# Kernel tuning notes

Measured on AMD Instinct MI355X. Metric: run time of the kernel, lower is better.

Reference implementation:

```python
import jax, jax.numpy as jnp
import numpy as np
import math

N_HEADS = 8
Q_DIM = 512          # number of query tokens (first Q_DIM rows of q)
INPUT_DIM = 512
EMBED_DIM = 512
HEAD_DIM = EMBED_DIM // N_HEADS  # key_dim == val_dim == 64
BATCH = 8
TOTAL_TOKENS = 4096  # Q_DIM queries + 3584 context tokens
NORM = 1.0 / math.sqrt(HEAD_DIM)


def setup_inputs() -> dict:
    key = jax.random.key(0)
    k1, k2, k3, k4, k5 = jax.random.split(key, 5)
    stdv = 1.0 / math.sqrt(HEAD_DIM)
    return {
        "q": jax.random.normal(k1, (BATCH, TOTAL_TOKENS, INPUT_DIM), dtype=jnp.float32),
        "W_query": jax.random.uniform(k2, (N_HEADS, INPUT_DIM, HEAD_DIM), minval=-stdv, maxval=stdv, dtype=jnp.float32),
        "W_key": jax.random.uniform(k3, (N_HEADS, INPUT_DIM, HEAD_DIM), minval=-stdv, maxval=stdv, dtype=jnp.float32),
        "W_val": jax.random.uniform(k4, (N_HEADS, INPUT_DIM, HEAD_DIM), minval=-stdv, maxval=stdv, dtype=jnp.float32),
        "W_out": jax.random.uniform(k5, (N_HEADS, HEAD_DIM, EMBED_DIM), minval=-1.0 / math.sqrt(EMBED_DIM), maxval=1.0 / math.sqrt(EMBED_DIM), dtype=jnp.float32),
    }


def reference(q, W_query, W_key, W_val, W_out):
    # Split packed input: first Q_DIM tokens are queries, rest are context.
    q_ = q[:, :Q_DIM, :]          # [b, nq, d_in]
    h = q[:, Q_DIM:, :]           # [b, g, d_in]
    Q = jnp.einsum('bqi,hik->hbqk', q_, W_query)   # [h, b, nq, dk]
    K = jnp.einsum('bgi,hik->hbgk', h, W_key)      # [h, b, g, dk]
    V = jnp.einsum('bgi,hiv->hbgv', h, W_val)      # [h, b, g, dv]
    compat = NORM * jnp.einsum('hbqk,hbgk->hbqg', Q, K)  # [h, b, nq, g]
    attn = jax.nn.softmax(compat, axis=-1)
    heads = jnp.einsum('hbqg,hbgv->hbqv', attn, V)       # [h, b, nq, dv]
    out = jnp.einsum('hbqv,hve->bqe', heads, W_out)      # [b, nq, embed]
    return out
```

## Files before the change

### kernel.cpp

```cpp
#include <hip/hip_runtime.h>

typedef _Float16 f16;
typedef _Float16 f16x4 __attribute__((ext_vector_type(4)));
typedef _Float16 f16x8 __attribute__((ext_vector_type(8)));
typedef float    f32x4 __attribute__((ext_vector_type(4)));

#define MFMA(a,b,c) __builtin_amdgcn_mfma_f32_16x16x32_f16(a,b,c,0,0,0)

#if __has_builtin(__builtin_amdgcn_exp2f)
#define EXP2(x) __builtin_amdgcn_exp2f(x)
#else
#define EXP2(x) exp2f(x)
#endif

__device__ __forceinline__ void gld16(const void* g, void* l) {
  typedef __attribute__((address_space(1))) unsigned GU;
  typedef __attribute__((address_space(3))) unsigned LU;
  __builtin_amdgcn_global_load_lds((GU*)g, (LU*)l, 16, 0, 0);
}

__global__ __launch_bounds__(256) void transp_w(
    const float* __restrict__ Wq, const float* __restrict__ Wk,
    const float* __restrict__ Wv, const float* __restrict__ Wo,
    f16* __restrict__ Wqt, f16* __restrict__ Wkt, f16* __restrict__ Wvt,
    f16* __restrict__ Wot)
{
  __shared__ float T[64 * 65];
  int bid = blockIdx.x, t = threadIdx.x;
  int mat = bid >> 6;
  int i0 = (bid & 7) * 64, c0 = ((bid >> 3) & 7) * 64;
  const float* src; f16* dst; float scale = 1.f;
  if      (mat == 0) { src = Wq; dst = Wqt; scale = 0.125f * 1.4426950408889634f; }
  else if (mat == 1) { src = Wk; dst = Wkt; }
  else if (mat == 2) { src = Wv; dst = Wvt; }
  else               { src = Wo; dst = Wot; }
#pragma unroll
  for (int p = 0; p < 4; ++p) {
    int row = p * 16 + (t >> 4), col = (t & 15) * 4;
    const float* a = (mat < 3)
        ? src + ((c0 >> 6) * 512 + i0 + row) * 64 + col
        : src + (i0 + row) * 512 + c0 + col;
    f32x4 v = *(const f32x4*)a;
    T[row * 65 + col + 0] = v[0] * scale;
    T[row * 65 + col + 1] = v[1] * scale;
    T[row * 65 + col + 2] = v[2] * scale;
    T[row * 65 + col + 3] = v[3] * scale;
  }
  __syncthreads();
#pragma unroll
  for (int p = 0; p < 16; ++p) {
    int cc = (t >> 6) * 16 + p, ii = t & 63;
    dst[(c0 + cc) * 512 + i0 + ii] = (f16)T[ii * 65 + cc];
  }
}

__global__ __launch_bounds__(256, 3) void proj_kernel(
    const float* __restrict__ q,
    const f16* __restrict__ Wqt, const f16* __restrict__ Wkt, const f16* __restrict__ Wvt,
    f16* __restrict__ Qh, f16* __restrict__ Kh, f16* __restrict__ Vtb)
{
  __shared__ f16 Asl[2][4096];
  __shared__ f16 Bsl[2][4096];

  int bid0 = blockIdx.x;
  int tile = (bid0 & 7) * 240 + (bid0 >> 3);

  int tid = threadIdx.x, l = tid & 63, w = tid >> 6;
  int wr = w >> 1, wc = w & 1;

  bool qmode = tile < 128;
  int rt, colbase, vmode = 0;
  const f16* Wt;
  if (qmode) {
    rt = tile >> 2; colbase = (tile & 3) * 128; Wt = Wqt;
  } else {
    int t2 = tile - 128; rt = t2 >> 3; int cc = t2 & 7;
    if (cc < 4) { Wt = Wkt; colbase = cc * 128; }
    else        { Wt = Wvt; colbase = (cc - 4) * 128; vmode = 1; }
  }
  int gbase, bidx;
  if (qmode) { bidx = rt >> 2; gbase = bidx * 4096 + (rt & 3) * 128; }
  else       { bidx = rt / 28; gbase = bidx * 4096 + 512 + (rt * 128 - bidx * 3584); }

  const float* asrc[2];
  const f16*   bsrc[2];
  int ldst[2];
#pragma unroll
  for (int j = 0; j < 2; ++j) {
    int s = tid + j * 256;
    int r = s >> 2;
    int c = (s & 3) ^ ((r >> 1) & 3);
    asrc[j] = q  + (size_t)(gbase + r) * 512 + c * 8;
    bsrc[j] = Wt + (size_t)(colbase + r) * 512 + c * 8;
    ldst[j] = (j * 256 + w * 64) * 8;
  }
  int awrow = tid >> 1, awh = tid & 1;
  int awo0 = awrow * 64 + (((awh * 2 + 0) ^ ((awrow >> 1) & 3)) << 4);
  int awo1 = awrow * 64 + (((awh * 2 + 1) ^ ((awrow >> 1) & 3)) << 4);
  const float* awsrc = q + (size_t)(gbase + awrow) * 512 + awh * 16;

  int aro[4], bro[4];
#pragma unroll
  for (int i = 0; i < 4; ++i) {
    int ra = wr * 64 + i * 16 + (l & 15);
    aro[i] = ra * 64 + ((((l >> 4)) ^ ((ra >> 1) & 3)) << 4);
    int rb = wc * 64 + i * 16 + (l & 15);
    bro[i] = rb * 64 + ((((l >> 4)) ^ ((rb >> 1) & 3)) << 4);
  }

  const f32x4 z4 = {0.f, 0.f, 0.f, 0.f};
  f32x4 acc[4][4];
#pragma unroll
  for (int i = 0; i < 4; ++i)
#pragma unroll
    for (int j = 0; j < 4; ++j) acc[i][j] = z4;

  f32x4 ar0, ar1, ar2, ar3;

  ar0 = *(const f32x4*)(awsrc + 0);
  ar1 = *(const f32x4*)(awsrc + 4);
  ar2 = *(const f32x4*)(awsrc + 8);
  ar3 = *(const f32x4*)(awsrc + 12);
  gld16(bsrc[0], &Bsl[0][ldst[0]]);
  gld16(bsrc[1], &Bsl[0][ldst[1]]);
  {
    f16x8 h0, h1;
#pragma unroll
    for (int e = 0; e < 4; ++e) { h0[e] = (f16)ar0[e]; h0[4+e] = (f16)ar1[e];
                                  h1[e] = (f16)ar2[e]; h1[4+e] = (f16)ar3[e]; }
    *(f16x8*)((char*)&Asl[0][0] + awo0) = h0;
    *(f16x8*)((char*)&Asl[0][0] + awo1) = h1;
  }
  __syncthreads();

  for (int ks = 0; ks < 16; ++ks) {
    int cur = ks & 1;
    if (ks < 15) {
      int k0 = (ks + 1) * 32;
      ar0 = *(const f32x4*)(awsrc + k0 + 0);
      ar1 = *(const f32x4*)(awsrc + k0 + 4);
      ar2 = *(const f32x4*)(awsrc + k0 + 8);
      ar3 = *(const f32x4*)(awsrc + k0 + 12);
      gld16(bsrc[0] + k0, &Bsl[cur ^ 1][ldst[0]]);
      gld16(bsrc[1] + k0, &Bsl[cur ^ 1][ldst[1]]);
    }
    const char* AB = (const char*)&Asl[cur][0];
    const char* BB = (const char*)&Bsl[cur][0];
    f16x8 af[4], bf[4];
#pragma unroll
    for (int i = 0; i < 4; ++i) af[i] = *(const f16x8*)(AB + aro[i]);
#pragma unroll
    for (int i = 0; i < 4; ++i) bf[i] = *(const f16x8*)(BB + bro[i]);
#pragma unroll
    for (int mi = 0; mi < 4; ++mi)
#pragma unroll
      for (int ni = 0; ni < 4; ++ni)
        acc[mi][ni] = MFMA(af[mi], bf[ni], acc[mi][ni]);
    if (ks < 15) {
      f16x8 h0, h1;
#pragma unroll
      for (int e = 0; e < 4; ++e) { h0[e] = (f16)ar0[e]; h0[4+e] = (f16)ar1[e];
                                    h1[e] = (f16)ar2[e]; h1[4+e] = (f16)ar3[e]; }
      *(f16x8*)((char*)&Asl[cur ^ 1][0] + awo0) = h0;
      *(f16x8*)((char*)&Asl[cur ^ 1][0] + awo1) = h1;
    }
    __syncthreads();
  }

  if (qmode) {
#pragma unroll
    for (int mi = 0; mi < 4; ++mi) {
      int row = rt * 128 + wr * 64 + mi * 16 + (l >> 4) * 4;
#pragma unroll
      for (int ni = 0; ni < 4; ++ni) {
        int col = colbase + wc * 64 + ni * 16 + (l & 15);
#pragma unroll
        for (int r = 0; r < 4; ++r)
          Qh[(size_t)(row + r) * 512 + col] = (f16)acc[mi][ni][r];
      }
    }
  } else if (!vmode) {
#pragma unroll
    for (int mi = 0; mi < 4; ++mi) {
      int row = rt * 128 + wr * 64 + mi * 16 + (l >> 4) * 4;
#pragma unroll
      for (int ni = 0; ni < 4; ++ni) {
        int col = colbase + wc * 64 + ni * 16 + (l & 15);
#pragma unroll
        for (int r = 0; r < 4; ++r)
          Kh[(size_t)(row + r) * 512 + col] = (f16)acc[mi][ni][r];
      }
    }
  } else {
    int g0 = rt * 128 - bidx * 3584;
#pragma unroll
    for (int mi = 0; mi < 4; ++mi) {
      int g = g0 + wr * 64 + mi * 16 + (l >> 4) * 4;
#pragma unroll
      for (int ni = 0; ni < 4; ++ni) {
        int c4 = colbase + wc * 64 + ni * 16 + (l & 15);
        int hh = c4 >> 6, v = c4 & 63;
        f16x4 o4;
        o4[0] = (f16)acc[mi][ni][0]; o4[1] = (f16)acc[mi][ni][1];
        o4[2] = (f16)acc[mi][ni][2]; o4[3] = (f16)acc[mi][ni][3];
        *(f16x4*)(Vtb + (size_t)((bidx * 8 + hh) * 64 + v) * 3584 + g) = o4;
      }
    }
  }
}

__global__ __launch_bounds__(512, 4) void attn_kernel(
    const f16* __restrict__ Qh, const f16* __restrict__ Kh,
    const f16* __restrict__ Vtb, f16* __restrict__ Opart,
    float* __restrict__ Ml, float* __restrict__ Ll)
{
  __shared__ f16 Klds[2][4096];
  __shared__ f16 Vlds[2][4096];
  __shared__ f16 Plds[8 * 1152];

  int bid = blockIdx.x;
  int seg = bid & 1, qt = (bid >> 1) & 3, h = (bid >> 3) & 7, bb = bid >> 6;
  int q0 = qt * 128;
  int tid = threadIdx.x, l = tid & 63, w = tid >> 6;

  f16x8 qf0, qf1;
  {
    int qrow = q0 + w * 16 + (l & 15);
    const f16* qb = Qh + (bb * 512 + qrow) * 512 + h * 64 + ((l >> 4) * 8);
    qf0 = *(const f16x8*)qb;
    qf1 = *(const f16x8*)(qb + 32);
  }

  bool isK = (w < 4);
  int sdo[2], ssrc[2];
#pragma unroll
  for (int j = 0; j < 2; ++j) {
    int id = (isK ? w : (w - 4)) * 2 + j;
    int rr = id * 8 + (l >> 3);
    int co = ((l & 7) ^ (rr & 7)) * 8;
    sdo[j] = id * 512;
    if (isK) ssrc[j] = (bb * 3584 + seg * 1792 + rr) * 512 + h * 64 + co;
    else     ssrc[j] = ((bb * 8 + h) * 64 + rr) * 3584 + seg * 1792 + co;
  }

  const f32x4 z4 = {0.f, 0.f, 0.f, 0.f};
  f32x4 acco[4];
#pragma unroll
  for (int i = 0; i < 4; ++i) acco[i] = z4;
  float mrow = -1e30f, lrow = 0.f;

  char* PwB = (char*)&Plds[w * 1152];
  int pwbase = (l & 15) * 144 + (l >> 4) * 8;
  int prbase = (l & 15) * 144 + (l >> 4) * 16;

  if (isK) { gld16(Kh + ssrc[0], &Klds[0][sdo[0]]); gld16(Kh + ssrc[1], &Klds[0][sdo[1]]); }
  else     { gld16(Vtb + ssrc[0], &Vlds[0][sdo[0]]); gld16(Vtb + ssrc[1], &Vlds[0][sdo[1]]); }
  __syncthreads();

  int buf = 0;
  for (int it = 0; it < 28; ++it) {
    if (it < 27) {
      int g0 = (it + 1) * 64;
      if (isK) { gld16(Kh + ssrc[0] + g0 * 512, &Klds[buf ^ 1][sdo[0]]);
                 gld16(Kh + ssrc[1] + g0 * 512, &Klds[buf ^ 1][sdo[1]]); }
      else     { gld16(Vtb + ssrc[0] + g0, &Vlds[buf ^ 1][sdo[0]]);
                 gld16(Vtb + ssrc[1] + g0, &Vlds[buf ^ 1][sdo[1]]); }
    }
    const char* KB = (const char*)&Klds[buf][0];
    const char* VB = (const char*)&Vlds[buf][0];

    f32x4 accs[4];
#pragma unroll
    for (int i = 0; i < 4; ++i) accs[i] = z4;
#pragma unroll
    for (int ni = 0; ni < 4; ++ni) {
      int g = ni * 16 + (l & 15);
      const char* rp = KB + g * 128;
      f16x8 k0 = *(const f16x8*)(rp + ((((l >> 4)    ) ^ (g & 7)) << 4));
      f16x8 k1 = *(const f16x8*)(rp + (((4 + (l >> 4)) ^ (g & 7)) << 4));
      accs[ni] = MFMA(k0, qf0, accs[ni]);
      accs[ni] = MFMA(k1, qf1, accs[ni]);
    }

    float n0 = fmaxf(fmaxf(accs[0][0], accs[0][1]), fmaxf(accs[0][2], accs[0][3]));
    float n1 = fmaxf(fmaxf(accs[1][0], accs[1][1]), fmaxf(accs[1][2], accs[1][3]));
    float n2 = fmaxf(fmaxf(accs[2][0], accs[2][1]), fmaxf(accs[2][2], accs[2][3]));
    float n3 = fmaxf(fmaxf(accs[3][0], accs[3][1]), fmaxf(accs[3][2], accs[3][3]));
    float tm = fmaxf(fmaxf(n0, n1), fmaxf(n2, n3));
    tm = fmaxf(tm, __shfl_xor(tm, 16));
    tm = fmaxf(tm, __shfl_xor(tm, 32));
    float mn = fmaxf(mrow, tm);
    float alpha = EXP2(mrow - mn);
    mrow = mn;

    float rs = 0.f;
#pragma unroll
    for (int ni = 0; ni < 4; ++ni) {
      float s0 = EXP2(accs[ni][0] - mrow);
      float s1 = EXP2(accs[ni][1] - mrow);
      float s2 = EXP2(accs[ni][2] - mrow);
      float s3 = EXP2(accs[ni][3] - mrow);
      rs += (s0 + s1) + (s2 + s3);
      f16x4 p4;
      p4[0] = (f16)s0; p4[1] = (f16)s1; p4[2] = (f16)s2; p4[3] = (f16)s3;
      *(f16x4*)(PwB + pwbase + ni * 32) = p4;
    }
    rs += __shfl_xor(rs, 16);
    rs += __shfl_xor(rs, 32);
    lrow = lrow * alpha + rs;
#pragma unroll
    for (int ni = 0; ni < 4; ++ni)
#pragma unroll
      for (int r = 0; r < 4; ++r) acco[ni][r] *= alpha;

    asm volatile("s_waitcnt lgkmcnt(0)" ::: "memory");

#pragma unroll
    for (int kc = 0; kc < 2; ++kc) {
      f16x8 pf = *(const f16x8*)(PwB + prbase + kc * 64);
#pragma unroll
      for (int ni = 0; ni < 4; ++ni) {
        int v = ni * 16 + (l & 15);
        f16x8 vf = *(const f16x8*)(VB + v * 128 + (((kc * 4 + (l >> 4)) ^ (v & 7)) << 4));
        acco[ni] = MFMA(vf, pf, acco[ni]);
      }
    }

    __syncthreads();
    buf ^= 1;
  }

  float inv = 1.f / lrow;
  int q = q0 + w * 16 + (l & 15);
  size_t obase = ((size_t)(seg * 64 + bb * 8 + h) * 512 + q) * 64;
#pragma unroll
  for (int ni = 0; ni < 4; ++ni) {
    f16x4 o4;
    o4[0] = (f16)(acco[ni][0] * inv); o4[1] = (f16)(acco[ni][1] * inv);
    o4[2] = (f16)(acco[ni][2] * inv); o4[3] = (f16)(acco[ni][3] * inv);
    *(f16x4*)(Opart + obase + ni * 16 + (l >> 4) * 4) = o4;
  }
  if ((l >> 4) == 0) {
    int mi = (seg * 64 + bb * 8 + h) * 512 + q;
    Ml[mi] = mrow; Ll[mi] = lrow;
  }
}

__global__ __launch_bounds__(256) void merge_kernel(
    const f16* __restrict__ Opart, const float* __restrict__ Ml,
    const float* __restrict__ Ll, f16* __restrict__ Hm)
{
  int row = blockIdx.x * 4 + (threadIdx.x >> 6);
  int l = threadIdx.x & 63;
  int bh = row >> 9, q = row & 511;
  int i0 = bh * 512 + q;
  int i1 = (64 + bh) * 512 + q;
  float o0 = (float)Opart[(size_t)i0 * 64 + l];
  float o1 = (float)Opart[(size_t)i1 * 64 + l];
  float m0 = Ml[i0], l0 = Ll[i0], m1 = Ml[i1], l1 = Ll[i1];
  float m = fmaxf(m0, m1);
  float w0 = EXP2(m0 - m) * l0, w1 = EXP2(m1 - m) * l1;
  float o = (w0 * o0 + w1 * o1) / (w0 + w1);
  int bb = bh >> 3, hh = bh & 7;
  Hm[((size_t)(bb * 512 + q)) * 512 + hh * 64 + l] = (f16)o;
}

__global__ __launch_bounds__(256) void outproj_kernel(
    const f16* __restrict__ Hm, const f16* __restrict__ Wot, float* __restrict__ out)
{
  __shared__ f16 Asl[2][4096];
  __shared__ f16 Bsl[2][4096];
  int bid = blockIdx.x;
  int rt = bid >> 2, ct = bid & 3;
  int tid = threadIdx.x, l = tid & 63, w = tid >> 6;
  int m0 = rt * 128, n0 = ct * 128;
  int wr = w >> 1, wc = w & 1;

  int an[2], aco[2];
#pragma unroll
  for (int j = 0; j < 2; ++j) {
    int r = (w * 2 + j) * 16 + (l >> 2);
    an[j] = r;
    aco[j] = ((l & 3) ^ (r & 3)) * 8;
  }

  const f32x4 z4 = {0.f, 0.f, 0.f, 0.f};
  f32x4 acc[4][4];
#pragma unroll
  for (int i = 0; i < 4; ++i)
#pragma unroll
    for (int jj = 0; jj < 4; ++jj) acc[i][jj] = z4;

  auto stage = [&](int bufi, int k0) {
#pragma unroll
    for (int j = 0; j < 2; ++j) {
      gld16(Hm  + (m0 + an[j]) * 512 + k0 + aco[j], &Asl[bufi][(w * 2 + j) * 512]);
      gld16(Wot + (n0 + an[j]) * 512 + k0 + aco[j], &Bsl[bufi][(w * 2 + j) * 512]);
    }
  };

  stage(0, 0);
  __syncthreads();
  for (int ks = 0; ks < 16; ++ks) {
    int bufi = ks & 1;
    if (ks < 15) stage(bufi ^ 1, (ks + 1) * 32);
    const char* AB = (const char*)&Asl[bufi][0];
    const char* BB = (const char*)&Bsl[bufi][0];
    f16x8 af[4], bf[4];
#pragma unroll
    for (int mi = 0; mi < 4; ++mi) {
      int row = wr * 64 + mi * 16 + (l & 15);
      af[mi] = *(const f16x8*)(AB + row * 64 + (((l >> 4) ^ (row & 3)) << 4));
    }
#pragma unroll
    for (int ni = 0; ni < 4; ++ni) {
      int rn = wc * 64 + ni * 16 + (l & 15);
      bf[ni] = *(const f16x8*)(BB + rn * 64 + (((l >> 4) ^ (rn & 3)) << 4));
    }
#pragma unroll
    for (int mi = 0; mi < 4; ++mi)
#pragma unroll
      for (int ni = 0; ni < 4; ++ni)
        acc[mi][ni] = MFMA(af[mi], bf[ni], acc[mi][ni]);
    __syncthreads();
  }

#pragma unroll
  for (int mi = 0; mi < 4; ++mi) {
    int row = m0 + wr * 64 + mi * 16 + (l >> 4) * 4;
#pragma unroll
    for (int ni = 0; ni < 4; ++ni) {
      int col = n0 + wc * 64 + ni * 16 + (l & 15);
#pragma unroll
      for (int r = 0; r < 4; ++r)
        out[(row + r) * 512 + col] = acc[mi][ni][r];
    }
  }
}

extern "C" void kernel_launch(void* const* d_in, const int* in_sizes, int n_in,
                              void* d_out, int out_size, void* d_ws, size_t ws_size,
                              hipStream_t stream) {
  const float* q  = (const float*)d_in[0];
  const float* Wq = (const float*)d_in[1];
  const float* Wk = (const float*)d_in[2];
  const float* Wv = (const float*)d_in[3];
  const float* Wo = (const float*)d_in[4];
  float* out = (float*)d_out;

  f16* ws  = (f16*)d_ws;
  f16* Wqt = ws;
  f16* Wkt = Wqt + 262144;
  f16* Wvt = Wkt + 262144;
  f16* Wot = Wvt + 262144;
  f16* Qh  = Wot + 262144;
  f16* Kh  = Qh  + 4096 * 512;
  f16* Vtb = Kh  + 28672 * 512;
  f16* Opart = Vtb + 28672 * 512;
  float* Ml = (float*)(Opart + 2 * 64 * 512 * 64);
  float* Ll = Ml + 65536;
  f16* Hm = Qh;

  transp_w<<<dim3(256),  dim3(256), 0, stream>>>(Wq, Wk, Wv, Wo, Wqt, Wkt, Wvt, Wot);
  proj_kernel<<<dim3(1920), dim3(256), 0, stream>>>(q, Wqt, Wkt, Wvt, Qh, Kh, Vtb);
  attn_kernel<<<dim3(512), dim3(512), 0, stream>>>(Qh, Kh, Vtb, Opart, Ml, Ll);
  merge_kernel<<<dim3(8192), dim3(256), 0, stream>>>(Opart, Ml, Ll, Hm);
  outproj_kernel<<<dim3(128), dim3(256), 0, stream>>>(Hm, Wot, out);
}
```

Baseline: 231.6 us.

## Deepen projection A-prefetch with fine waitcnt and split attention into four KV segments

After: 243.4 us. 1.05x slower.

```diff
diff --git a/kernel.cpp b/kernel.cpp
--- a/kernel.cpp
+++ b/kernel.cpp
@@ -12,6 +12,8 @@
 #else
 #define EXP2(x) exp2f(x)
 #endif
+
+#define SBAR() __builtin_amdgcn_sched_barrier(0)
 
 __device__ __forceinline__ void gld16(const void* g, void* l) {
   typedef __attribute__((address_space(1))) unsigned GU;
@@ -82,15 +84,13 @@
   if (qmode) { bidx = rt >> 2; gbase = bidx * 4096 + (rt & 3) * 128; }
   else       { bidx = rt / 28; gbase = bidx * 4096 + 512 + (rt * 128 - bidx * 3584); }
 
-  const float* asrc[2];
-  const f16*   bsrc[2];
+  const f16* bsrc[2];
   int ldst[2];
 #pragma unroll
   for (int j = 0; j < 2; ++j) {
     int s = tid + j * 256;
     int r = s >> 2;
     int c = (s & 3) ^ ((r >> 1) & 3);
-    asrc[j] = q  + (size_t)(gbase + r) * 512 + c * 8;
     bsrc[j] = Wt + (size_t)(colbase + r) * 512 + c * 8;
     ldst[j] = (j * 256 + w * 64) * 8;
   }
@@ -115,56 +115,71 @@
 #pragma unroll
     for (int j = 0; j < 4; ++j) acc[i][j] = z4;
 
-  f32x4 ar0, ar1, ar2, ar3;
-
-  ar0 = *(const f32x4*)(awsrc + 0);
-  ar1 = *(const f32x4*)(awsrc + 4);
-  ar2 = *(const f32x4*)(awsrc + 8);
-  ar3 = *(const f32x4*)(awsrc + 12);
+  f32x4 ar[2][4];
+
+  auto awrite = [&](int bank, int bufi) {
+    f16x8 h0, h1;
+#pragma unroll
+    for (int e = 0; e < 4; ++e) {
+      h0[e] = (f16)ar[bank][0][e]; h0[4 + e] = (f16)ar[bank][1][e];
+      h1[e] = (f16)ar[bank][2][e]; h1[4 + e] = (f16)ar[bank][3][e];
+    }
+    *(f16x8*)((char*)&Asl[bufi][0] + awo0) = h0;
+    *(f16x8*)((char*)&Asl[bufi][0] + awo1) = h1;
+  };
+
+#pragma unroll
+  for (int i = 0; i < 4; ++i) ar[0][i] = *(const f32x4*)(awsrc + i * 4);
+  SBAR();
+  awrite(0, 0);
+  SBAR();
   gld16(bsrc[0], &Bsl[0][ldst[0]]);
   gld16(bsrc[1], &Bsl[0][ldst[1]]);
-  {
-    f16x8 h0, h1;
-#pragma unroll
-    for (int e = 0; e < 4; ++e) { h0[e] = (f16)ar0[e]; h0[4+e] = (f16)ar1[e];
-                                  h1[e] = (f16)ar2[e]; h1[4+e] = (f16)ar3[e]; }
-    *(f16x8*)((char*)&Asl[0][0] + awo0) = h0;
-    *(f16x8*)((char*)&Asl[0][0] + awo1) = h1;
-  }
-  __syncthreads();
-
+  SBAR();
+#pragma unroll
+  for (int i = 0; i < 4; ++i) ar[1][i] = *(const f32x4*)(awsrc + 32 + i * 4);
+  SBAR();
+  asm volatile("s_waitcnt vmcnt(4) lgkmcnt(0)" ::: "memory");
+  __builtin_amdgcn_s_barrier();
+  SBAR();
+
+#pragma unroll
   for (int ks = 0; ks < 16; ++ks) {
-    int cur = ks & 1;
+    const int cur = ks & 1;
     if (ks < 15) {
-      int k0 = (ks + 1) * 32;
-      ar0 = *(const f32x4*)(awsrc + k0 + 0);
-      ar1 = *(const f32x4*)(awsrc + k0 + 4);
-      ar2 = *(const f32x4*)(awsrc + k0 + 8);
-      ar3 = *(const f32x4*)(awsrc + k0 + 12);
-      gld16(bsrc[0] + k0, &Bsl[cur ^ 1][ldst[0]]);
-      gld16(bsrc[1] + k0, &Bsl[cur ^ 1][ldst[1]]);
-    }
-    const char* AB = (const char*)&Asl[cur][0];
-    const char* BB = (const char*)&Bsl[cur][0];
-    f16x8 af[4], bf[4];
-#pragma unroll
-    for (int i = 0; i < 4; ++i) af[i] = *(const f16x8*)(AB + aro[i]);
-#pragma unroll
-    for (int i = 0; i < 4; ++i) bf[i] = *(const f16x8*)(BB + bro[i]);
-#pragma unroll
-    for (int mi = 0; mi < 4; ++mi)
-#pragma unroll
-      for (int ni = 0; ni < 4; ++ni)
-        acc[mi][ni] = MFMA(af[mi], bf[ni], acc[mi][ni]);
+      gld16(bsrc[0] + (ks + 1) * 32, &Bsl[cur ^ 1][ldst[0]]);
+      gld16(bsrc[1] + (ks + 1) * 32, &Bsl[cur ^ 1][ldst[1]]);
+    }
+    SBAR();
+    if (ks < 14) {
+#pragma unroll
+      for (int i = 0; i < 4; ++i)
+        ar[cur][i] = *(const f32x4*)(awsrc + (ks + 2) * 32 + i * 4);
+    }
+    SBAR();
+    {
+      const char* AB = (const char*)&Asl[cur][0];
+      const char* BB = (const char*)&Bsl[cur][0];
+      f16x8 af[4], bf[4];
+#pragma unroll
+      for (int i = 0; i < 4; ++i) af[i] = *(const f16x8*)(AB + aro[i]);
+#pragma unroll
+      for (int i = 0; i < 4; ++i) bf[i] = *(const f16x8*)(BB + bro[i]);
+#pragma unroll
+      for (int mi = 0; mi < 4; ++mi)
+#pragma unroll
+        for (int ni = 0; ni < 4; ++ni)
+          acc[mi][ni] = MFMA(af[mi], bf[ni], acc[mi][ni]);
+    }
+    SBAR();
     if (ks < 15) {
-      f16x8 h0, h1;
-#pragma unroll
-      for (int e = 0; e < 4; ++e) { h0[e] = (f16)ar0[e]; h0[4+e] = (f16)ar1[e];
-                                    h1[e] = (f16)ar2[e]; h1[4+e] = (f16)ar3[e]; }
-      *(f16x8*)((char*)&Asl[cur ^ 1][0] + awo0) = h0;
-      *(f16x8*)((char*)&Asl[cur ^ 1][0] + awo1) = h1;
-    }
-    __syncthreads();
+      awrite(cur ^ 1, cur ^ 1);
+      SBAR();
+      if (ks < 14) asm volatile("s_waitcnt vmcnt(4) lgkmcnt(0)" ::: "memory");
+      else         asm volatile("s_waitcnt vmcnt(0) lgkmcnt(0)" ::: "memory");
+      __builtin_amdgcn_s_barrier();
+      SBAR();
+    }
   }
 
   if (qmode) {
@@ -219,7 +234,7 @@
   __shared__ f16 Plds[8 * 1152];
 
   int bid = blockIdx.x;
-  int seg = bid & 1, qt = (bid >> 1) & 3, h = (bid >> 3) & 7, bb = bid >> 6;
+  int seg = bid & 3, qt = (bid >> 2) & 3, h = (bid >> 4) & 7, bb = bid >> 7;
   int q0 = qt * 128;
   int tid = threadIdx.x, l = tid & 63, w = tid >> 6;
 
@@ -239,8 +254,8 @@
     int rr = id * 8 + (l >> 3);
     int co = ((l & 7) ^ (rr & 7)) * 8;
     sdo[j] = id * 512;
-    if (isK) ssrc[j] = (bb * 3584 + seg * 1792 + rr) * 512 + h * 64 + co;
-    else     ssrc[j] = ((bb * 8 + h) * 64 + rr) * 3584 + seg * 1792 + co;
+    if (isK) ssrc[j] = (bb * 3584 + seg * 896 + rr) * 512 + h * 64 + co;
+    else     ssrc[j] = ((bb * 8 + h) * 64 + rr) * 3584 + seg * 896 + co;
   }
 
   const f32x4 z4 = {0.f, 0.f, 0.f, 0.f};
@@ -258,8 +273,8 @@
   __syncthreads();
 
   int buf = 0;
-  for (int it = 0; it < 28; ++it) {
-    if (it < 27) {
+  for (int it = 0; it < 14; ++it) {
+    if (it < 13) {
       int g0 = (it + 1) * 64;
       if (isK) { gld16(Kh + ssrc[0] + g0 * 512, &Klds[buf ^ 1][sdo[0]]);
                  gld16(Kh + ssrc[1] + g0 * 512, &Klds[buf ^ 1][sdo[1]]); }
@@ -353,16 +368,23 @@
   int row = blockIdx.x * 4 + (threadIdx.x >> 6);
   int l = threadIdx.x & 63;
   int bh = row >> 9, q = row & 511;
-  int i0 = bh * 512 + q;
-  int i1 = (64 + bh) * 512 + q;
-  float o0 = (float)Opart[(size_t)i0 * 64 + l];
-  float o1 = (float)Opart[(size_t)i1 * 64 + l];
-  float m0 = Ml[i0], l0 = Ll[i0], m1 = Ml[i1], l1 = Ll[i1];
-  float m = fmaxf(m0, m1);
-  float w0 = EXP2(m0 - m) * l0, w1 = EXP2(m1 - m) * l1;
-  float o = (w0 * o0 + w1 * o1) / (w0 + w1);
+  int idx[4];
+  float ms[4], ls[4], os[4];
+#pragma unroll
+  for (int s = 0; s < 4; ++s) {
+    idx[s] = (s * 64 + bh) * 512 + q;
+    ms[s] = Ml[idx[s]]; ls[s] = Ll[idx[s]];
+    os[s] = (float)Opart[(size_t)idx[s] * 64 + l];
+  }
+  float m = fmaxf(fmaxf(ms[0], ms[1]), fmaxf(ms[2], ms[3]));
+  float num = 0.f, den = 0.f;
+#pragma unroll
+  for (int s = 0; s < 4; ++s) {
+    float ws = EXP2(ms[s] - m) * ls[s];
+    num += ws * os[s]; den += ws;
+  }
   int bb = bh >> 3, hh = bh & 7;
-  Hm[((size_t)(bb * 512 + q)) * 512 + hh * 64 + l] = (f16)o;
+  Hm[((size_t)(bb * 512 + q)) * 512 + hh * 64 + l] = (f16)(num / den);
 }
 
 __global__ __launch_bounds__(256) void outproj_kernel(
@@ -457,13 +479,13 @@
   f16* Kh  = Qh  + 4096 * 512;
   f16* Vtb = Kh  + 28672 * 512;
   f16* Opart = Vtb + 28672 * 512;
-  float* Ml = (float*)(Opart + 2 * 64 * 512 * 64);
-  float* Ll = Ml + 65536;
+  float* Ml = (float*)(Opart + (size_t)4 * 64 * 512 * 64);
+  float* Ll = Ml + 131072;
   f16* Hm = Qh;
 
   transp_w<<<dim3(256),  dim3(256), 0, stream>>>(Wq, Wk, Wv, Wo, Wqt, Wkt, Wvt, Wot);
   proj_kernel<<<dim3(1920), dim3(256), 0, stream>>>(q, Wqt, Wkt, Wvt, Qh, Kh, Vtb);
-  attn_kernel<<<dim3(512), dim3(512), 0, stream>>>(Qh, Kh, Vtb, Opart, Ml, Ll);
+  attn_kernel<<<dim3(1024), dim3(512), 0, stream>>>(Qh, Kh, Vtb, Opart, Ml, Ll);
   merge_kernel<<<dim3(8192), dim3(256), 0, stream>>>(Opart, Ml, Ll, Hm);
   outproj_kernel<<<dim3(128), dim3(256), 0, stream>>>(Hm, Wot, out);
 }
```

## Split attention context into four segments and halve out-projection row tiles

Applied to the files above, without the earlier changes.

Measured after the change: 267.9 us. 1.16x slower.

```diff
diff --git a/kernel.cpp b/kernel.cpp
--- a/kernel.cpp
+++ b/kernel.cpp
@@ -54,7 +54,7 @@
   }
 }
 
-__global__ __launch_bounds__(256, 3) void proj_kernel(
+__global__ __launch_bounds__(256, 5) void proj_kernel(
     const float* __restrict__ q,
     const f16* __restrict__ Wqt, const f16* __restrict__ Wkt, const f16* __restrict__ Wvt,
     f16* __restrict__ Qh, f16* __restrict__ Kh, f16* __restrict__ Vtb)
@@ -82,15 +82,13 @@
   if (qmode) { bidx = rt >> 2; gbase = bidx * 4096 + (rt & 3) * 128; }
   else       { bidx = rt / 28; gbase = bidx * 4096 + 512 + (rt * 128 - bidx * 3584); }
 
-  const float* asrc[2];
-  const f16*   bsrc[2];
+  const f16* bsrc[2];
   int ldst[2];
 #pragma unroll
   for (int j = 0; j < 2; ++j) {
     int s = tid + j * 256;
     int r = s >> 2;
     int c = (s & 3) ^ ((r >> 1) & 3);
-    asrc[j] = q  + (size_t)(gbase + r) * 512 + c * 8;
     bsrc[j] = Wt + (size_t)(colbase + r) * 512 + c * 8;
     ldst[j] = (j * 256 + w * 64) * 8;
   }
@@ -219,7 +217,7 @@
   __shared__ f16 Plds[8 * 1152];
 
   int bid = blockIdx.x;
-  int seg = bid & 1, qt = (bid >> 1) & 3, h = (bid >> 3) & 7, bb = bid >> 6;
+  int seg = bid & 3, qt = (bid >> 2) & 3, h = (bid >> 4) & 7, bb = bid >> 7;
   int q0 = qt * 128;
   int tid = threadIdx.x, l = tid & 63, w = tid >> 6;
 
@@ -239,8 +237,8 @@
     int rr = id * 8 + (l >> 3);
     int co = ((l & 7) ^ (rr & 7)) * 8;
     sdo[j] = id * 512;
-    if (isK) ssrc[j] = (bb * 3584 + seg * 1792 + rr) * 512 + h * 64 + co;
-    else     ssrc[j] = ((bb * 8 + h) * 64 + rr) * 3584 + seg * 1792 + co;
+    if (isK) ssrc[j] = (bb * 3584 + seg * 896 + rr) * 512 + h * 64 + co;
+    else     ssrc[j] = ((bb * 8 + h) * 64 + rr) * 3584 + seg * 896 + co;
   }
 
   const f32x4 z4 = {0.f, 0.f, 0.f, 0.f};
@@ -258,8 +256,8 @@
   __syncthreads();
 
   int buf = 0;
-  for (int it = 0; it < 28; ++it) {
-    if (it < 27) {
+  for (int it = 0; it < 14; ++it) {
+    if (it < 13) {
       int g0 = (it + 1) * 64;
       if (isK) { gld16(Kh + ssrc[0] + g0 * 512, &Klds[buf ^ 1][sdo[0]]);
                  gld16(Kh + ssrc[1] + g0 * 512, &Klds[buf ^ 1][sdo[1]]); }
@@ -353,50 +351,69 @@
   int row = blockIdx.x * 4 + (threadIdx.x >> 6);
   int l = threadIdx.x & 63;
   int bh = row >> 9, q = row & 511;
-  int i0 = bh * 512 + q;
-  int i1 = (64 + bh) * 512 + q;
-  float o0 = (float)Opart[(size_t)i0 * 64 + l];
-  float o1 = (float)Opart[(size_t)i1 * 64 + l];
-  float m0 = Ml[i0], l0 = Ll[i0], m1 = Ml[i1], l1 = Ll[i1];
-  float m = fmaxf(m0, m1);
-  float w0 = EXP2(m0 - m) * l0, w1 = EXP2(m1 - m) * l1;
-  float o = (w0 * o0 + w1 * o1) / (w0 + w1);
+  int idx[4];
+  float ms[4], ls[4], os[4];
+#pragma unroll
+  for (int s = 0; s < 4; ++s) {
+    idx[s] = (s * 64 + bh) * 512 + q;
+    ms[s] = Ml[idx[s]]; ls[s] = Ll[idx[s]];
+    os[s] = (float)Opart[(size_t)idx[s] * 64 + l];
+  }
+  float m = fmaxf(fmaxf(ms[0], ms[1]), fmaxf(ms[2], ms[3]));
+  float num = 0.f, den = 0.f;
+#pragma unroll
+  for (int s = 0; s < 4; ++s) {
+    float ws = EXP2(ms[s] - m) * ls[s];
+    num += ws * os[s]; den += ws;
+  }
   int bb = bh >> 3, hh = bh & 7;
-  Hm[((size_t)(bb * 512 + q)) * 512 + hh * 64 + l] = (f16)o;
-}
-
-__global__ __launch_bounds__(256) void outproj_kernel(
+  Hm[((size_t)(bb * 512 + q)) * 512 + hh * 64 + l] = (f16)(num / den);
+}
+
+__global__ __launch_bounds__(256, 2) void outproj_kernel(
     const f16* __restrict__ Hm, const f16* __restrict__ Wot, float* __restrict__ out)
 {
-  __shared__ f16 Asl[2][4096];
+  __shared__ f16 Asl[2][2048];
   __shared__ f16 Bsl[2][4096];
   int bid = blockIdx.x;
   int rt = bid >> 2, ct = bid & 3;
   int tid = threadIdx.x, l = tid & 63, w = tid >> 6;
-  int m0 = rt * 128, n0 = ct * 128;
+  int m0 = rt * 64, n0 = ct * 128;
   int wr = w >> 1, wc = w & 1;
 
-  int an[2], aco[2];
+  int ra_ = tid >> 2, ca_ = (tid & 3) ^ ((ra_ >> 1) & 3);
+  const f16* asrc = Hm + (size_t)(m0 + ra_) * 512 + ca_ * 8;
+  int adst = (w * 64) * 8;
+  const f16* bsrc[2]; int bdst[2];
 #pragma unroll
   for (int j = 0; j < 2; ++j) {
-    int r = (w * 2 + j) * 16 + (l >> 2);
-    an[j] = r;
-    aco[j] = ((l & 3) ^ (r & 3)) * 8;
+    int s = tid + j * 256, r = s >> 2, c = (s & 3) ^ ((r >> 1) & 3);
+    bsrc[j] = Wot + (size_t)(n0 + r) * 512 + c * 8;
+    bdst[j] = (j * 256 + w * 64) * 8;
+  }
+  int aro[2], bro[4];
+#pragma unroll
+  for (int i = 0; i < 2; ++i) {
+    int ra = wr * 32 + i * 16 + (l & 15);
+    aro[i] = ra * 64 + ((((l >> 4)) ^ ((ra >> 1) & 3)) << 4);
+  }
+#pragma unroll
+  for (int i = 0; i < 4; ++i) {
+    int rb = wc * 64 + i * 16 + (l & 15);
+    bro[i] = rb * 64 + ((((l >> 4)) ^ ((rb >> 1) & 3)) << 4);
   }
 
   const f32x4 z4 = {0.f, 0.f, 0.f, 0.f};
-  f32x4 acc[4][4];
-#pragma unroll
-  for (int i = 0; i < 4; ++i)
+  f32x4 acc[2][4];
+#pragma unroll
+  for (int i = 0; i < 2; ++i)
 #pragma unroll
     for (int jj = 0; jj < 4; ++jj) acc[i][jj] = z4;
 
   auto stage = [&](int bufi, int k0) {
-#pragma unroll
-    for (int j = 0; j < 2; ++j) {
-      gld16(Hm  + (m0 + an[j]) * 512 + k0 + aco[j], &Asl[bufi][(w * 2 + j) * 512]);
-      gld16(Wot + (n0 + an[j]) * 512 + k0 + aco[j], &Bsl[bufi][(w * 2 + j) * 512]);
-    }
+    gld16(asrc + k0, &Asl[bufi][adst]);
+    gld16(bsrc[0] + k0, &Bsl[bufi][bdst[0]]);
+    gld16(bsrc[1] + k0, &Bsl[bufi][bdst[1]]);
   };
 
   stage(0, 0);
@@ -406,19 +423,13 @@
     if (ks < 15) stage(bufi ^ 1, (ks + 1) * 32);
     const char* AB = (const char*)&Asl[bufi][0];
     const char* BB = (const char*)&Bsl[bufi][0];
-    f16x8 af[4], bf[4];
-#pragma unroll
-    for (int mi = 0; mi < 4; ++mi) {
-      int row = wr * 64 + mi * 16 + (l & 15);
-      af[mi] = *(const f16x8*)(AB + row * 64 + (((l >> 4) ^ (row & 3)) << 4));
-    }
-#pragma unroll
-    for (int ni = 0; ni < 4; ++ni) {
-      int rn = wc * 64 + ni * 16 + (l & 15);
-      bf[ni] = *(const f16x8*)(BB + rn * 64 + (((l >> 4) ^ (rn & 3)) << 4));
-    }
-#pragma unroll
-    for (int mi = 0; mi < 4; ++mi)
+    f16x8 af[2], bf[4];
+#pragma unroll
+    for (int i = 0; i < 2; ++i) af[i] = *(const f16x8*)(AB + aro[i]);
+#pragma unroll
+    for (int i = 0; i < 4; ++i) bf[i] = *(const f16x8*)(BB + bro[i]);
+#pragma unroll
+    for (int mi = 0; mi < 2; ++mi)
 #pragma unroll
       for (int ni = 0; ni < 4; ++ni)
         acc[mi][ni] = MFMA(af[mi], bf[ni], acc[mi][ni]);
@@ -426,14 +437,14 @@
   }
 
 #pragma unroll
-  for (int mi = 0; mi < 4; ++mi) {
-    int row = m0 + wr * 64 + mi * 16 + (l >> 4) * 4;
+  for (int mi = 0; mi < 2; ++mi) {
+    int row = m0 + wr * 32 + mi * 16 + (l >> 4) * 4;
 #pragma unroll
     for (int ni = 0; ni < 4; ++ni) {
       int col = n0 + wc * 64 + ni * 16 + (l & 15);
 #pragma unroll
       for (int r = 0; r < 4; ++r)
-        out[(row + r) * 512 + col] = acc[mi][ni][r];
+        out[(size_t)(row + r) * 512 + col] = acc[mi][ni][r];
     }
   }
 }
@@ -457,13 +468,13 @@
   f16* Kh  = Qh  + 4096 * 512;
   f16* Vtb = Kh  + 28672 * 512;
   f16* Opart = Vtb + 28672 * 512;
-  float* Ml = (float*)(Opart + 2 * 64 * 512 * 64);
-  float* Ll = Ml + 65536;
+  float* Ml = (float*)(Opart + (size_t)4 * 64 * 512 * 64);
+  float* Ll = Ml + 131072;
   f16* Hm = Qh;
 
   transp_w<<<dim3(256),  dim3(256), 0, stream>>>(Wq, Wk, Wv, Wo, Wqt, Wkt, Wvt, Wot);
   proj_kernel<<<dim3(1920), dim3(256), 0, stream>>>(q, Wqt, Wkt, Wvt, Qh, Kh, Vtb);
-  attn_kernel<<<dim3(512), dim3(512), 0, stream>>>(Qh, Kh, Vtb, Opart, Ml, Ll);
+  attn_kernel<<<dim3(1024), dim3(512), 0, stream>>>(Qh, Kh, Vtb, Opart, Ml, Ll);
   merge_kernel<<<dim3(8192), dim3(256), 0, stream>>>(Opart, Ml, Ll, Hm);
-  outproj_kernel<<<dim3(128), dim3(256), 0, stream>>>(Hm, Wot, out);
-}
+  outproj_kernel<<<dim3(256), dim3(256), 0, stream>>>(Hm, Wot, out);
+}
```
